# Kernel optimization log

Hardware: AMD Instinct MI355X
Metric: run time of the kernel (lower is better)

## Reference

```python
import jax, jax.numpy as jnp
import numpy as np

N_HASHES = 4
CHUNK = 144
REDUCTION = 4

# PyTorch bicubic (a=-0.75), align_corners=False, integer scale 2 ->
# fixed fractional offsets t=0.75 (even outputs) and t=0.25 (odd outputs).
_EW = jnp.array([-0.03515625, 0.26171875, 0.87890625, -0.10546875], jnp.float32)
_OW = _EW[::-1]


def _up2_axis(x, axis):
    n = x.shape[axis]
    pad = [(0, 0)] * x.ndim
    pad[axis] = (2, 2)
    xp = jnp.pad(x, pad, mode='edge')  # torch clamps border indices
    sl = lambda s: jax.lax.slice_in_dim(xp, s, s + n, axis=axis)
    even = sum(_EW[k] * sl(k) for k in range(4))
    odd = sum(_OW[k] * sl(k + 1) for k in range(4))
    out = jnp.stack([even, odd], axis=axis + 1)
    shp = list(x.shape)
    shp[axis] = 2 * n
    return out.reshape(shp)


def bicubic_up2(x):
    return _up2_axis(_up2_axis(x, 2), 3)


def conv2d(x, w, b, pad):
    y = jax.lax.conv_general_dilated(x, w, (1, 1), [(pad, pad), (pad, pad)],
                                     dimension_numbers=('NCHW', 'OIHW', 'NCHW'))
    return y + b[None, :, None, None]


def _adj(t):
    # attend to own + two adjacent buckets along chunk axis (axis=2)
    return jnp.concatenate([t, jnp.roll(t, 1, axis=2), jnp.roll(t, -1, axis=2)], axis=3)


def nlsa(x, wm, bm, wa, ba, rot):
    N, Cc, H, W = x.shape
    L = H * W
    xe = conv2d(x, wm, bm, 1).reshape(N, -1, L).transpose(0, 2, 1)  # [N,L,C]
    ye = conv2d(x, wa, ba, 0).reshape(N, -1, L).transpose(0, 2, 1)  # [N,L,C*red]
    C = xe.shape[-1]
    hash_buckets = min(L // CHUNK + (L // CHUNK) % 2, 128)
    # LSH: random rotations -> argmax bucket codes (non-differentiable, detached)
    rotated = jnp.einsum('btf,fhi->bhti', xe, rot)  # [N,h,L,hb//2]
    rotated = jnp.concatenate([rotated, -rotated], axis=-1)  # [N,h,L,hb]
    codes = jnp.argmax(rotated, axis=-1)  # [N,h,L]
    codes = codes + (jnp.arange(N_HASHES) * hash_buckets)[None, :, None]
    codes = jax.lax.stop_gradient(codes.reshape(N, -1))  # [N,h*L]
    indices = jnp.argsort(codes, axis=-1)
    undo = jnp.argsort(indices, axis=-1)
    mod = indices % L
    xs = jnp.take_along_axis(xe, mod[..., None], axis=1)  # [N,h*L,C]
    ys = jnp.take_along_axis(ye, mod[..., None], axis=1)  # [N,h*L,C*red]
    padding = (-L) % CHUNK
    xb = xs.reshape(N, N_HASHES, L, C)
    yb = ys.reshape(N, N_HASHES, L, C * REDUCTION)
    if padding:
        xb = jnp.concatenate([xb, xb[:, :, -padding:, :]], axis=2)
        yb = jnp.concatenate([yb, yb[:, :, -padding:, :]], axis=2)
    nch = xb.shape[2] // CHUNK
    xb = xb.reshape(N, N_HASHES, nch, CHUNK, C)
    yb = yb.reshape(N, N_HASHES, nch, CHUNK, C * REDUCTION)
    xm = xb / jnp.maximum(jnp.linalg.norm(xb, axis=-1, keepdims=True), 5e-5)
    xm = _adj(xm)      # [N,h,k,3*chunk,C]
    ybj = _adj(yb)     # [N,h,k,3*chunk,C*red]
    raw = jnp.einsum('bhkie,bhkje->bhkij', xb, xm)  # [N,h,k,chunk,3*chunk]
    bscore = jax.scipy.special.logsumexp(raw, axis=-1, keepdims=True)
    score = jnp.exp(raw - bscore)
    ret = jnp.einsum('bhkij,bhkje->bhkie', score, ybj)
    ret = ret.reshape(N, N_HASHES, -1, C * REDUCTION)
    bscore = bscore.reshape(N, N_HASHES, -1)
    if padding:
        ret = ret[:, :, :-padding]
        bscore = bscore[:, :, :-padding]
    ret = ret.reshape(N, -1, C * REDUCTION)
    bscore = bscore.reshape(N, -1)
    ret = jnp.take_along_axis(ret, undo[..., None], axis=1)
    bscore = jnp.take_along_axis(bscore, undo, axis=1)
    ret = ret.reshape(N, N_HASHES, L, C * REDUCTION)
    probs = jax.nn.softmax(bscore.reshape(N, N_HASHES, L, 1), axis=1)
    ret = jnp.sum(ret * probs, axis=1)  # [N,L,C*red]
    return ret.transpose(0, 2, 1).reshape(N, -1, H, W) + x


def setup_inputs() -> dict:
    key = jax.random.key(0)
    ks = jax.random.split(key, 8)
    w = lambda k, shape, fan: (jax.random.normal(k, shape, jnp.float32) / np.sqrt(fan)).astype(jnp.float32)
    return {
        'x': jax.random.normal(ks[0], (2, 64, 96, 96), jnp.float32),
        'w1': w(ks[1], (64, 64, 3, 3), 64 * 9), 'b1': jnp.zeros((64,), jnp.float32),
        'w2': w(ks[2], (64, 64, 3, 3), 64 * 9), 'b2': jnp.zeros((64,), jnp.float32),
        'wm': w(ks[3], (16, 64, 3, 3), 64 * 9), 'bm': jnp.zeros((16,), jnp.float32),
        'wa': w(ks[4], (64, 64, 1, 1), 64), 'ba': jnp.zeros((64,), jnp.float32),
        'rot': jax.random.normal(ks[5], (16, N_HASHES, 64), jnp.float32),  # [C, h, hash_buckets//2]
    }


def reference(x, w1, b1, w2, b2, wm, bm, wa, ba, rot):
    x = bicubic_up2(x)
    x = jax.nn.relu(conv2d(x, w1, b1, 1))
    x = jax.nn.relu(conv2d(x, w2, b2, 1))
    return nlsa(x, wm, bm, wa, ba, rot)
```

## Files before the change

kernel.cpp:

```cpp
#include <hip/hip_runtime.h>
#include <math.h>

#define NB 2
#define CIN 64
#define H0 96
#define W0 96
#define HH 192
#define WW 192
#define LL (HH*WW)
#define NHASH 4
#define CHK 144
#define NCHK 256
#define CE 16
#define CV 64
#define NBUCK 128
#define SEGL 576
#define NSEG 64

#define K_ROWB   80
#define V_ROWB   912
#define P_ROWB   72
#define KQ_SZB   34560
#define VT_SZB   58368
#define PST_SZB  10368
#define LKI_SZB  1728
#define QN_SZB   576
#define LDS_T1   (VT_SZB + PST_SZB + LKI_SZB)
#define LDS_T2   (KQ_SZB + VT_SZB + PST_SZB + LKI_SZB + QN_SZB)
#define CONV_LDS (2*4*66*64*2)

typedef __attribute__((ext_vector_type(8))) short short8_t;
typedef __attribute__((ext_vector_type(4))) float f32x4;
union FragU { unsigned int u[4]; int4 i; short8_t s; };

__device__ __forceinline__ unsigned int cvtpk_bf16(float a, float b){
  unsigned int r;
  asm("v_cvt_pk_bf16_f32 %0, %1, %2" : "=v"(r) : "v"(a), "v"(b));
  return r;
}
__device__ __forceinline__ float bfl(unsigned int u){ return __uint_as_float(u << 16); }
__device__ __forceinline__ float bfh(unsigned int u){ return __uint_as_float(u & 0xffff0000u); }

__global__ __launch_bounds__(256) void k_upsample(const float* __restrict__ x,
                                                  float* __restrict__ out){
  int idx = blockIdx.x*256 + threadIdx.x;
  if (idx >= NB*CIN*HH*WW) return;
  int ox = idx % WW; int t2 = idx / WW;
  int oy = t2 % HH;  t2 /= HH;
  int i = oy >> 1, a = oy & 1;
  int j = ox >> 1, b = ox & 1;
  const float e0=-0.03515625f, e1=0.26171875f, e2=0.87890625f, e3=-0.10546875f;
  float wy[4], wx[4]; int ty[4], tx[4];
  if (a){ wy[0]=e3; wy[1]=e2; wy[2]=e1; wy[3]=e0; } else { wy[0]=e0; wy[1]=e1; wy[2]=e2; wy[3]=e3; }
  if (b){ wx[0]=e3; wx[1]=e2; wx[2]=e1; wx[3]=e0; } else { wx[0]=e0; wx[1]=e1; wx[2]=e2; wx[3]=e3; }
  int offy = a ? -1 : -2, offx = b ? -1 : -2;
  #pragma unroll
  for (int k=0;k<4;k++){
    int t = i + offy + k; ty[k] = t<0?0:(t>H0-1?H0-1:t);
    int s = j + offx + k; tx[k] = s<0?0:(s>W0-1?W0-1:s);
  }
  const float* xp = x + (size_t)t2*H0*W0;
  float s = 0.f;
  #pragma unroll
  for (int ky=0;ky<4;ky++){
    const float* row = xp + ty[ky]*W0;
    float rs = 0.f;
    rs = fmaf(wx[0], row[tx[0]], rs);
    rs = fmaf(wx[1], row[tx[1]], rs);
    rs = fmaf(wx[2], row[tx[2]], rs);
    rs = fmaf(wx[3], row[tx[3]], rs);
    s = fmaf(wy[ky], rs, s);
  }
  out[idx] = s;
}

__global__ __launch_bounds__(256) void k_prepw(const float* __restrict__ w,
    unsigned short* __restrict__ wsT, int CO){
  int idx = blockIdx.x*256 + threadIdx.x;
  if (idx >= CO*64*9) return;
  int tap = idx % 9; int rem = idx / 9;
  int ci = rem % 64; int co = rem / 64;
  float v = w[(size_t)(co*64 + ci)*9 + tap];
  unsigned int hu = cvtpk_bf16(v, v) & 0xffffu;
  float hf = bfl(hu);
  unsigned int lu = cvtpk_bf16(v - hf, 0.f) & 0xffffu;
  int half = ci >> 5, kg = (ci >> 3) & 3, e = ci & 7;
  size_t base = ((size_t)(tap*2 + half)*2)*CO*32 + ((size_t)co*4 + kg)*8 + e;
  wsT[base]         = (unsigned short)hu;
  wsT[base + (size_t)CO*32] = (unsigned short)lu;
}

template<int CO, bool RELU, bool OUT_NLC>
__global__ __launch_bounds__(256) void k_conv3m(const float* __restrict__ in,
    const unsigned short* __restrict__ wsT, const float* __restrict__ bias,
    float* __restrict__ out){
  extern __shared__ char cvsm[];
  unsigned short (*inH)[66][64] = (unsigned short (*)[66][64])cvsm;
  unsigned short (*inL)[66][64] = (unsigned short (*)[66][64])(cvsm + 4*66*64*2);
  const int t = threadIdx.x;
  const int bx = blockIdx.x, by = blockIdx.y, n = blockIdx.z;
  const int y0 = by*2;
  const int x0 = bx*64;
  const int l = t & 63, w = t >> 6;
  const int lq = l & 15, kg = l >> 4;

  for (int e = t; e < 4096; e += 256){
    const int chunk = e & 15;
    const int strip = e >> 4;
    const int ci = strip & 63, row = strip >> 6;
    const int gy = y0 + row - 1;
    float4 v = make_float4(0.f,0.f,0.f,0.f);
    if (gy >= 0 && gy < HH)
      v = *(const float4*)&in[(((size_t)n*CIN + ci)*HH + gy)*WW + x0 + chunk*4];
    float vv[4] = {v.x, v.y, v.z, v.w};
    #pragma unroll
    for (int j = 0; j < 4; ++j){
      const int col = 1 + chunk*4 + j;
      const int sci = (((ci >> 3) ^ (col & 7)) << 3) | (ci & 7);
      unsigned int hu = cvtpk_bf16(vv[j], vv[j]);
      unsigned int lu = cvtpk_bf16(vv[j] - bfl(hu), 0.f);
      inH[row][col][sci] = (unsigned short)hu;
      inL[row][col][sci] = (unsigned short)lu;
    }
  }
  {
    const int ci = t & 63, row = t >> 6;
    const int gy = y0 + row - 1;
    const bool okY = (gy >= 0 && gy < HH);
    const float* ip = &in[(((size_t)n*CIN + ci)*HH + (size_t)(okY?gy:0))*WW];
    float vL = (okY && x0 >= 1) ? ip[x0-1] : 0.f;
    float vR = (okY && x0+64 < WW) ? ip[x0+64] : 0.f;
    unsigned int hL = cvtpk_bf16(vL, vL);
    unsigned int lLu = cvtpk_bf16(vL - bfl(hL), 0.f);
    unsigned int hR = cvtpk_bf16(vR, vR);
    unsigned int lRu = cvtpk_bf16(vR - bfl(hR), 0.f);
    const int sci0 = ci;
    const int sci65 = (((ci >> 3) ^ 1) << 3) | (ci & 7);
    inH[row][0][sci0]  = (unsigned short)hL;  inL[row][0][sci0]  = (unsigned short)lLu;
    inH[row][65][sci65] = (unsigned short)hR; inL[row][65][sci65] = (unsigned short)lRu;
  }
  __syncthreads();

  constexpr int NCT = CO/16;
  f32x4 acc0[NCT], acc1[NCT];
  #pragma unroll
  for (int c=0;c<NCT;c++){ acc0[c] = (f32x4){0.f,0.f,0.f,0.f}; acc1[c] = acc0[c]; }
  const unsigned short* wlane = wsT + (size_t)lq*32 + (size_t)kg*8;

  #pragma unroll
  for (int tap=0; tap<9; ++tap){
    const int ky = tap/3, kx = tap - ky*3;
    const int col = w*16 + lq + kx;
    #pragma unroll
    for (int half=0; half<2; ++half){
      const int sci = ((((half<<2) | kg) ^ (col & 7)) << 3);
      FragU Bh0, Bl0, Bh1, Bl1;
      Bh0.i = *(const int4*)&inH[ky  ][col][sci];
      Bl0.i = *(const int4*)&inL[ky  ][col][sci];
      Bh1.i = *(const int4*)&inH[ky+1][col][sci];
      Bl1.i = *(const int4*)&inL[ky+1][col][sci];
      const unsigned short* wth = wlane + (size_t)((tap*2+half)*2)*CO*32;
      #pragma unroll
      for (int ct=0; ct<NCT; ++ct){
        FragU Ah, Al;
        Ah.i = *(const int4*)(wth + ct*512);
        Al.i = *(const int4*)(wth + CO*32 + ct*512);
        acc0[ct] = __builtin_amdgcn_mfma_f32_16x16x32_bf16(Ah.s, Bl0.s, acc0[ct], 0,0,0);
        acc0[ct] = __builtin_amdgcn_mfma_f32_16x16x32_bf16(Al.s, Bh0.s, acc0[ct], 0,0,0);
        acc0[ct] = __builtin_amdgcn_mfma_f32_16x16x32_bf16(Ah.s, Bh0.s, acc0[ct], 0,0,0);
        acc1[ct] = __builtin_amdgcn_mfma_f32_16x16x32_bf16(Ah.s, Bl1.s, acc1[ct], 0,0,0);
        acc1[ct] = __builtin_amdgcn_mfma_f32_16x16x32_bf16(Al.s, Bh1.s, acc1[ct], 0,0,0);
        acc1[ct] = __builtin_amdgcn_mfma_f32_16x16x32_bf16(Ah.s, Bh1.s, acc1[ct], 0,0,0);
      }
    }
  }

  const int px = x0 + w*16 + lq;
  if constexpr (!OUT_NLC){
    #pragma unroll
    for (int ct=0; ct<NCT; ++ct){
      #pragma unroll
      for (int r=0; r<4; ++r){
        const int co = ct*16 + kg*4 + r;
        const float bv = bias[co];
        float v0 = acc0[ct][r] + bv;
        float v1 = acc1[ct][r] + bv;
        if (RELU){ v0 = fmaxf(v0, 0.f); v1 = fmaxf(v1, 0.f); }
        out[(((size_t)n*CO + co)*HH + y0  )*WW + px] = v0;
        out[(((size_t)n*CO + co)*HH + y0+1)*WW + px] = v1;
      }
    }
  } else {
    #pragma unroll
    for (int r=0; r<4; ++r){
      const int co = kg*4 + r;
      const float bv = bias[co];
      float v0 = acc0[0][r] + bv;
      float v1 = acc1[0][r] + bv;
      if (RELU){ v0 = fmaxf(v0, 0.f); v1 = fmaxf(v1, 0.f); }
      out[((size_t)n*LL + (y0  )*WW + px)*CO + co] = v0;
      out[((size_t)n*LL + (y0+1)*WW + px)*CO + co] = v1;
    }
  }
}

__global__ __launch_bounds__(256) void k_conv1x1(const float* __restrict__ x2,
    const float* __restrict__ wa, const float* __restrict__ ba,
    unsigned short* __restrict__ yeB){
  __shared__ float xs[64][64];
  __shared__ float wts[64][64];
  const int t = threadIdx.x;
  const int n = blockIdx.y;
  const int l0 = blockIdx.x*64;
  for (int e=t; e<4096; e+=256){
    int ci = e >> 6, l = e & 63;
    xs[ci][l]  = x2[((size_t)n*CIN+ci)*LL + l0 + l];
    wts[ci][l] = wa[(size_t)l*64 + ci];
  }
  __syncthreads();
  const int l = t & 63, cq = t >> 6;
  float acc[16];
  #pragma unroll
  for (int i=0;i<16;i++) acc[i] = ba[cq*16+i];
  for (int ci=0; ci<64; ci++){
    float xv = xs[ci][l];
    #pragma unroll
    for (int i=0;i<16;i++) acc[i] = fmaf(xv, wts[ci][cq*16+i], acc[i]);
  }
  unsigned int wds[8];
  #pragma unroll
  for (int i=0;i<8;i++) wds[i] = cvtpk_bf16(acc[2*i], acc[2*i+1]);
  uint4* op = (uint4*)&yeB[((size_t)n*LL + l0 + l)*64 + cq*16];
  op[0] = make_uint4(wds[0],wds[1],wds[2],wds[3]);
  op[1] = make_uint4(wds[4],wds[5],wds[6],wds[7]);
}

__global__ __launch_bounds__(128) void k_codes(const float* __restrict__ xe,
    const float* __restrict__ rot, unsigned char* __restrict__ codes){
  __shared__ float rs[NHASH][64][16];
  const int t = threadIdx.x;
  for (int e=t; e<4096; e+=128){
    int f = e >> 8; int rem = e & 255;
    int h = rem >> 6; int i = rem & 63;
    rs[h][i][f] = rot[((size_t)f*NHASH + h)*64 + i];
  }
  __syncthreads();
  const int n = blockIdx.y;
  const int l = blockIdx.x*128 + t;
  float q[16];
  const float* xr = &xe[((size_t)n*LL + l)*16];
  #pragma unroll
  for (int f=0;f<16;f++) q[f] = xr[f];
  #pragma unroll
  for (int h=0;h<NHASH;h++){
    float bp = -3.0e38f, bn = -3.0e38f; int ap=0, an=0;
    for (int i=0;i<64;i++){
      float s = 0.f;
      #pragma unroll
      for (int f=0;f<16;f++) s = fmaf(q[f], rs[h][i][f], s);
      if (s > bp){ bp = s; ap = i; }
      if (-s > bn){ bn = -s; an = i; }
    }
    int code = (bp >= bn) ? ap : (64 + an);
    codes[((size_t)n*NHASH + h)*LL + l] = (unsigned char)code;
  }
}

__global__ __launch_bounds__(256) void k_hist(const unsigned char* __restrict__ codes,
    unsigned int* __restrict__ segHist){
  __shared__ unsigned int h[NBUCK];
  const int t = threadIdx.x;
  if (t < NBUCK) h[t] = 0;
  __syncthreads();
  const int n = blockIdx.z, hh = blockIdx.y, s = blockIdx.x;
  const unsigned char* cp = codes + ((size_t)n*NHASH + hh)*LL + (size_t)s*SEGL;
  for (int e=t; e<SEGL; e+=256) atomicAdd(&h[cp[e]], 1u);
  __syncthreads();
  if (t < NBUCK)
    segHist[(((size_t)(n*NHASH+hh))*NSEG + s)*NBUCK + t] = h[t];
}

__global__ __launch_bounds__(128) void k_scan(unsigned int* __restrict__ segHist){
  __shared__ unsigned int tot[NBUCK];
  __shared__ unsigned int base[NBUCK];
  const int b = threadIdx.x;
  const size_t off = (size_t)blockIdx.x * NSEG * NBUCK;
  unsigned int run = 0;
  for (int s=0;s<NSEG;s++){
    unsigned int v = segHist[off + (size_t)s*NBUCK + b];
    segHist[off + (size_t)s*NBUCK + b] = run;
    run += v;
  }
  tot[b] = run;
  __syncthreads();
  if (b==0){ unsigned int r=0; for (int i=0;i<NBUCK;i++){ base[i]=r; r+=tot[i]; } }
  __syncthreads();
  const unsigned int bb = base[b];
  for (int s=0;s<NSEG;s++) segHist[off + (size_t)s*NBUCK + b] += bb;
}

__global__ __launch_bounds__(256) void k_rank(const unsigned char* __restrict__ codes,
    const unsigned int* __restrict__ segHist, int* __restrict__ sortPos,
    int* __restrict__ srtIdx){
  __shared__ unsigned int cw[SEGL/4];
  __shared__ unsigned int sbase[NBUCK];
  const int t = threadIdx.x;
  const int n = blockIdx.z, hh = blockIdx.y, s = blockIdx.x;
  const size_t cb = ((size_t)n*NHASH + hh)*LL + (size_t)s*SEGL;
  const unsigned int* cp32 = (const unsigned int*)(codes + cb);
  for (int e=t; e<SEGL/4; e+=256) cw[e] = cp32[e];
  if (t < NBUCK)
    sbase[t] = segHist[(((size_t)(n*NHASH+hh))*NSEG + s)*NBUCK + t];
  __syncthreads();
  const size_t ob = ((size_t)n*NHASH + hh)*LL;
  for (int e=t; e<SEGL; e+=256){
    unsigned int c = (cw[e>>2] >> ((e&3)*8)) & 0xffu;
    unsigned int mul = c * 0x01010101u;
    int cnt = 0;
    const int nw = e >> 2;
    for (int wi=0; wi<nw; wi++){
      unsigned int v = cw[wi] ^ mul;
      unsigned int t1 = (v & 0x7f7f7f7fu) + 0x7f7f7f7fu;
      unsigned int z = ~(t1 | v) & 0x80808080u;
      cnt += __popc(z);
    }
    unsigned int lastw = cw[nw];
    const int nbp = e & 3;
    for (int bp=0; bp<nbp; bp++)
      if (((lastw >> (bp*8)) & 0xffu) == c) cnt++;
    int pos = (int)sbase[c] + cnt;
    int l = s*SEGL + e;
    sortPos[ob + l] = pos;
    srtIdx[ob + pos] = l;
  }
}

__global__ __launch_bounds__(256) void k_gatherK(const float* __restrict__ xe,
    const int* __restrict__ srtIdx, unsigned short* __restrict__ Ksrt,
    float* __restrict__ normQ){
  const int idx = blockIdx.x*256 + threadIdx.x;
  if (idx >= NB*NHASH*LL) return;
  const int n = idx / (NHASH*LL);
  const int lk = srtIdx[idx];
  const float4* xr = (const float4*)&xe[((size_t)n*LL + lk)*16];
  float4 v0 = xr[0], v1 = xr[1], v2 = xr[2], v3 = xr[3];
  float f[16] = {v0.x,v0.y,v0.z,v0.w, v1.x,v1.y,v1.z,v1.w,
                 v2.x,v2.y,v2.z,v2.w, v3.x,v3.y,v3.z,v3.w};
  float ss = 0.f;
  #pragma unroll
  for (int i=0;i<16;i++) ss = fmaf(f[i], f[i], ss);
  const float nq = sqrtf(ss);
  normQ[idx] = nq;
  const float inv = 1.f / fmaxf(nq, 5e-5f);
  #pragma unroll
  for (int i=0;i<16;i++) f[i] *= inv;
  unsigned int kh[8], klo[8];
  #pragma unroll
  for (int i=0;i<8;i++) kh[i] = cvtpk_bf16(f[2*i], f[2*i+1]);
  #pragma unroll
  for (int i=0;i<8;i++)
    klo[i] = cvtpk_bf16(f[2*i] - bfl(kh[i]), f[2*i+1] - bfh(kh[i]));
  int4* kr = (int4*)(Ksrt + (size_t)idx*32);
  kr[0] = make_int4((int)kh[0],(int)kh[1],(int)kh[2],(int)kh[3]);
  kr[1] = make_int4((int)kh[4],(int)kh[5],(int)kh[6],(int)kh[7]);
  kr[2] = make_int4((int)klo[0],(int)klo[1],(int)klo[2],(int)klo[3]);
  kr[3] = make_int4((int)klo[4],(int)klo[5],(int)klo[6],(int)klo[7]);
}

template<int TIER>
__global__ __launch_bounds__(576) void k_attn2(const float* __restrict__ xe,
    const unsigned short* __restrict__ yeB, const int* __restrict__ srtIdx,
    const unsigned short* __restrict__ Ksrt, const float* __restrict__ normQ,
    unsigned short* __restrict__ retS, float* __restrict__ bscore){
  extern __shared__ char smem[];
  constexpr int KQOFF = (TIER==2) ? KQ_SZB : 0;
  unsigned short* Kq = (unsigned short*)smem;
  char* Vt  = smem + KQOFF;
  char* Pst = Vt + VT_SZB;
  int* lkI  = (int*)(Pst + PST_SZB);
  float* qn = (float*)(Pst + PST_SZB + LKI_SZB);

  const int t = threadIdx.x;
  const int k = blockIdx.x, hh = blockIdx.y, n = blockIdx.z;
  const size_t sb = ((size_t)n*NHASH + hh)*LL;
  const int l = t & 63, w = t >> 6;
  const int lq16 = l & 15, g = l >> 4;

  if (t < 432){
    const int c3 = t / CHK, jl = t - c3*CHK;
    const int kc = (c3==0) ? k : ((c3==1) ? ((k+NCHK-1)&(NCHK-1)) : ((k+1)&(NCHK-1)));
    const int lk = srtIdx[sb + (size_t)kc*CHK + jl];
    lkI[t] = lk;
    if constexpr (TIER==2){
      const float4* xr = (const float4*)&xe[((size_t)n*LL + lk)*16];
      float4 v0 = xr[0], v1 = xr[1], v2 = xr[2], v3 = xr[3];
      float f[16] = {v0.x,v0.y,v0.z,v0.w, v1.x,v1.y,v1.z,v1.w,
                     v2.x,v2.y,v2.z,v2.w, v3.x,v3.y,v3.z,v3.w};
      float ss = 0.f;
      #pragma unroll
      for (int i=0;i<16;i++) ss = fmaf(f[i], f[i], ss);
      const float nq = sqrtf(ss);
      if (c3 == 0) qn[jl] = nq;
      const float inv = 1.f / fmaxf(nq, 5e-5f);
      #pragma unroll
      for (int i=0;i<16;i++) f[i] *= inv;
      unsigned int kh[8], klo[8];
      #pragma unroll
      for (int i=0;i<8;i++) kh[i] = cvtpk_bf16(f[2*i], f[2*i+1]);
      #pragma unroll
      for (int i=0;i<8;i++)
        klo[i] = cvtpk_bf16(f[2*i] - bfl(kh[i]), f[2*i+1] - bfh(kh[i]));
      int4* kr = (int4*)((char*)Kq + t*K_ROWB);
      kr[0] = make_int4((int)kh[0],(int)kh[1],(int)kh[2],(int)kh[3]);
      kr[1] = make_int4((int)kh[4],(int)kh[5],(int)kh[6],(int)kh[7]);
      kr[2] = make_int4((int)klo[0],(int)klo[1],(int)klo[2],(int)klo[3]);
      kr[3] = make_int4((int)klo[4],(int)klo[5],(int)klo[6],(int)klo[7]);
    }
  }
  if (t < 512){
    int c = t >> 3, jp = t & 7;
    *(unsigned int*)(Vt + c*V_ROWB + 864 + jp*4) = 0u;
  }
  __syncthreads();

  #pragma unroll 4
  for (int it=0; it<24; ++it){
    const int e = t + it*576;
    const int jp = e >> 6, c = e & 63;
    const unsigned int a = yeB[((size_t)n*LL + lkI[2*jp  ])*64 + c];
    const unsigned int b = yeB[((size_t)n*LL + lkI[2*jp+1])*64 + c];
    *(unsigned int*)(Vt + c*V_ROWB + jp*4) = a | (b << 16);
  }
  const int qg = w*16 + lq16;
  const int pq = k*CHK + qg;
  FragU b1, b2;
  float nq_;
  if constexpr (TIER==1){
    const unsigned short* qrow = Ksrt + (sb + pq)*32;
    b1.i = *(const int4*)(qrow + (g&1)*8);
    if (g < 2) b2.i = *(const int4*)(qrow + 16 + (g&1)*8);
    else { b2.u[0]=0u; b2.u[1]=0u; b2.u[2]=0u; b2.u[3]=0u; }
    nq_ = normQ[sb + pq];
  } else {
    const char* qrow = (const char*)Kq + qg*K_ROWB;
    b1.i = *(const int4*)(qrow + (g&1)*16);
    if (g < 2) b2.i = *(const int4*)(qrow + 32 + (g&1)*16);
    else { b2.u[0]=0u; b2.u[1]=0u; b2.u[2]=0u; b2.u[3]=0u; }
    nq_ = qn[qg];
  }
  const float msc = fmaxf(nq_, 5e-5f);
  __syncthreads();

  float sum = 0.f;
  f32x4 O0 = {0.f,0.f,0.f,0.f}, O1 = O0, O2 = O0, O3 = O0;
  char* Pw = Pst + w*(16*P_ROWB);
  for (int u=0; u<14; ++u){
    #pragma unroll
    for (int sub=0; sub<2; ++sub){
      const int t27 = u*2 + sub;
      uint2 pw;
      if (t27 < 27){
        FragU a;
        if constexpr (TIER==1){
          const int c3 = t27 / 9;
          const int kc = (c3==0) ? k : ((c3==1) ? ((k+NCHK-1)&(NCHK-1)) : ((k+1)&(NCHK-1)));
          const int row16 = (t27 - c3*9)*16;
          a.i = *(const int4*)(Ksrt + (sb + (size_t)kc*CHK + row16 + lq16)*32 + g*8);
        } else {
          a.i = *(const int4*)((const char*)Kq + (size_t)(t27*16 + lq16)*K_ROWB + g*16);
        }
        f32x4 C = {0.f,0.f,0.f,0.f};
        C = __builtin_amdgcn_mfma_f32_16x16x32_bf16(a.s, b2.s, C, 0, 0, 0);
        C = __builtin_amdgcn_mfma_f32_16x16x32_bf16(a.s, b1.s, C, 0, 0, 0);
        const float p0 = __expf(fmaf(msc, C[0], -nq_));
        const float p1 = __expf(fmaf(msc, C[1], -nq_));
        const float p2 = __expf(fmaf(msc, C[2], -nq_));
        const float p3 = __expf(fmaf(msc, C[3], -nq_));
        sum += (p0+p1) + (p2+p3);
        pw = make_uint2(cvtpk_bf16(p0,p1), cvtpk_bf16(p2,p3));
      } else {
        pw = make_uint2(0u, 0u);
      }
      *(uint2*)(Pw + lq16*P_ROWB + sub*32 + g*8) = pw;
    }
    asm volatile("s_waitcnt lgkmcnt(0)" ::: "memory");
    __builtin_amdgcn_sched_barrier(0);
    FragU bp; bp.i = *(const int4*)(Pw + lq16*P_ROWB + g*16);
    const char* Vb = Vt + lq16*V_ROWB + u*64 + g*16;
    FragU av;
    av.i = *(const int4*)(Vb);             O0 = __builtin_amdgcn_mfma_f32_16x16x32_bf16(av.s, bp.s, O0, 0,0,0);
    av.i = *(const int4*)(Vb + 16*V_ROWB); O1 = __builtin_amdgcn_mfma_f32_16x16x32_bf16(av.s, bp.s, O1, 0,0,0);
    av.i = *(const int4*)(Vb + 32*V_ROWB); O2 = __builtin_amdgcn_mfma_f32_16x16x32_bf16(av.s, bp.s, O2, 0,0,0);
    av.i = *(const int4*)(Vb + 48*V_ROWB); O3 = __builtin_amdgcn_mfma_f32_16x16x32_bf16(av.s, bp.s, O3, 0,0,0);
  }
  sum += __shfl_xor(sum, 16);
  sum += __shfl_xor(sum, 32);
  const float linv = 1.f / sum;

  unsigned short* op = &retS[(sb + pq)*64];
  {
    uint2 s0 = make_uint2(cvtpk_bf16(O0[0]*linv, O0[1]*linv), cvtpk_bf16(O0[2]*linv, O0[3]*linv));
    uint2 s1 = make_uint2(cvtpk_bf16(O1[0]*linv, O1[1]*linv), cvtpk_bf16(O1[2]*linv, O1[3]*linv));
    uint2 s2 = make_uint2(cvtpk_bf16(O2[0]*linv, O2[1]*linv), cvtpk_bf16(O2[2]*linv, O2[3]*linv));
    uint2 s3 = make_uint2(cvtpk_bf16(O3[0]*linv, O3[1]*linv), cvtpk_bf16(O3[2]*linv, O3[3]*linv));
    *(uint2*)(op +  0 + g*4) = s0;
    *(uint2*)(op + 16 + g*4) = s1;
    *(uint2*)(op + 32 + g*4) = s2;
    *(uint2*)(op + 48 + g*4) = s3;
  }
  if (g == 0) bscore[sb + pq] = nq_ + logf(sum);
}

__global__ __launch_bounds__(256) void k_combine(const unsigned short* __restrict__ retS,
    const float* __restrict__ bscore, const int* __restrict__ sortPos,
    const float* __restrict__ x2, float* __restrict__ out){
  const int idx = blockIdx.x*256 + threadIdx.x;
  if (idx >= NB*LL) return;
  const int l = idx % LL, n = idx / LL;
  float bs[NHASH]; int pp[NHASH];
  #pragma unroll
  for (int h=0;h<NHASH;h++){
    size_t sb = ((size_t)n*NHASH + h)*LL;
    int p = sortPos[sb + l];
    pp[h] = p; bs[h] = bscore[sb + p];
  }
  float m = fmaxf(fmaxf(bs[0],bs[1]), fmaxf(bs[2],bs[3]));
  float wsum = 0.f; float wv[NHASH];
  #pragma unroll
  for (int h=0;h<NHASH;h++){ wv[h] = expf(bs[h]-m); wsum += wv[h]; }
  const float winv = 1.f / wsum;
  float o[64];
  #pragma unroll
  for (int i=0;i<64;i++) o[i]=0.f;
  #pragma unroll
  for (int h=0;h<NHASH;h++){
    const float wh = wv[h]*winv;
    const uint4* rp = (const uint4*)&retS[(((size_t)n*NHASH + h)*LL + pp[h])*64];
    #pragma unroll
    for (int i2=0;i2<8;i2++){
      uint4 v = rp[i2];
      o[i2*8+0] = fmaf(wh, bfl(v.x), o[i2*8+0]);
      o[i2*8+1] = fmaf(wh, bfh(v.x), o[i2*8+1]);
      o[i2*8+2] = fmaf(wh, bfl(v.y), o[i2*8+2]);
      o[i2*8+3] = fmaf(wh, bfh(v.y), o[i2*8+3]);
      o[i2*8+4] = fmaf(wh, bfl(v.z), o[i2*8+4]);
      o[i2*8+5] = fmaf(wh, bfh(v.z), o[i2*8+5]);
      o[i2*8+6] = fmaf(wh, bfl(v.w), o[i2*8+6]);
      o[i2*8+7] = fmaf(wh, bfh(v.w), o[i2*8+7]);
    }
  }
  #pragma unroll
  for (int c=0;c<64;c++){
    size_t oi = ((size_t)n*64 + c)*LL + l;
    out[oi] = o[c] + x2[oi];
  }
}

extern "C" void kernel_launch(void* const* d_in, const int* in_sizes, int n_in,
                              void* d_out, int out_size, void* d_ws, size_t ws_size,
                              hipStream_t stream){
  const float* x   = (const float*)d_in[0];
  const float* w1  = (const float*)d_in[1];
  const float* b1  = (const float*)d_in[2];
  const float* w2  = (const float*)d_in[3];
  const float* b2  = (const float*)d_in[4];
  const float* wm  = (const float*)d_in[5];
  const float* bm  = (const float*)d_in[6];
  const float* wa  = (const float*)d_in[7];
  const float* ba  = (const float*)d_in[8];
  const float* rot = (const float*)d_in[9];
  float* outp = (float*)d_out;
  char* ws = (char*)d_ws;
  const size_t FM   = (size_t)NB*CIN*HH*WW*sizeof(float);
  const size_t YEB  = (size_t)NB*LL*64*2;
  const size_t RETB = (size_t)NB*NHASH*LL*64*2;
  const size_t NHL4 = (size_t)NB*NHASH*LL*4;

  char* p = ws;
  unsigned short* yeB = (unsigned short*)p;  p += YEB;
  char* regA = p;                            p += RETB;
  float* x2  = (float*)p;                    p += FM;
  float* xe  = (float*)p;                    p += (size_t)NB*LL*CE*sizeof(float);
  unsigned char* codes = (unsigned char*)p;  p += (size_t)NB*NHASH*LL;
  unsigned int* segHist = (unsigned int*)p;  p += (size_t)NB*NHASH*NSEG*NBUCK*4;
  int* sortPos = (int*)p;                    p += NHL4;
  int* srtIdx  = (int*)p;                    p += NHL4;
  float* bscore = (float*)p;                 p += NHL4;
  unsigned short* wsT1 = (unsigned short*)p; p += (size_t)9*2*2*64*32*2;
  unsigned short* wsT2 = (unsigned short*)p; p += (size_t)9*2*2*64*32*2;
  unsigned short* wsTm = (unsigned short*)p; p += (size_t)9*2*2*16*32*2;
  const size_t needT2 = (size_t)(p - ws);
  unsigned short* Ksrt = (unsigned short*)p; p += (size_t)NB*NHASH*LL*32*2;
  float* normQ = (float*)p;                  p += NHL4;
  const size_t needT1 = (size_t)(p - ws);

  unsigned short* retS = (unsigned short*)regA;
  float* x0u = (float*)regA;
  float* y1  = (float*)(regA + FM);
  if (ws_size < needT2) return;
  const bool preg = (ws_size >= needT1);

  hipFuncSetAttribute((const void*)k_attn2<1>,
                      hipFuncAttributeMaxDynamicSharedMemorySize, LDS_T1);
  hipFuncSetAttribute((const void*)k_attn2<2>,
                      hipFuncAttributeMaxDynamicSharedMemorySize, LDS_T2);
  hipFuncSetAttribute((const void*)k_conv3m<64,true,false>,
                      hipFuncAttributeMaxDynamicSharedMemorySize, CONV_LDS);
  hipFuncSetAttribute((const void*)k_conv3m<16,false,true>,
                      hipFuncAttributeMaxDynamicSharedMemorySize, CONV_LDS);

  k_prepw<<<dim3((64*64*9+255)/256), dim3(256), 0, stream>>>(w1, wsT1, 64);
  k_prepw<<<dim3((64*64*9+255)/256), dim3(256), 0, stream>>>(w2, wsT2, 64);
  k_prepw<<<dim3((16*64*9+255)/256), dim3(256), 0, stream>>>(wm, wsTm, 16);
  k_upsample<<<dim3((NB*CIN*HH*WW+255)/256), dim3(256), 0, stream>>>(x, x0u);
  k_conv3m<64,true,false><<<dim3(3, HH/2, NB), dim3(256), CONV_LDS, stream>>>(x0u, wsT1, b1, y1);
  k_conv3m<64,true,false><<<dim3(3, HH/2, NB), dim3(256), CONV_LDS, stream>>>(y1, wsT2, b2, x2);
  k_conv3m<16,false,true><<<dim3(3, HH/2, NB), dim3(256), CONV_LDS, stream>>>(x2, wsTm, bm, xe);
  k_conv1x1<<<dim3(LL/64, NB), dim3(256), 0, stream>>>(x2, wa, ba, yeB);
  k_codes<<<dim3(LL/128, NB), dim3(128), 0, stream>>>(xe, rot, codes);
  k_hist<<<dim3(NSEG, NHASH, NB), dim3(256), 0, stream>>>(codes, segHist);
  k_scan<<<dim3(NB*NHASH), dim3(128), 0, stream>>>(segHist);
  k_rank<<<dim3(NSEG, NHASH, NB), dim3(256), 0, stream>>>(codes, segHist, sortPos, srtIdx);
  if (preg){
    k_gatherK<<<dim3((NB*NHASH*LL+255)/256), dim3(256), 0, stream>>>(xe, srtIdx, Ksrt, normQ);
    k_attn2<1><<<dim3(NCHK, NHASH, NB), dim3(576), LDS_T1, stream>>>(
        xe, yeB, srtIdx, Ksrt, normQ, retS, bscore);
  } else {
    k_attn2<2><<<dim3(NCHK, NHASH, NB), dim3(576), LDS_T2, stream>>>(
        xe, yeB, srtIdx, Ksrt, normQ, retS, bscore);
  }
  k_combine<<<dim3((NB*LL+255)/256), dim3(256), 0, stream>>>(retS, bscore, sortPos, x2, outp);
}
```

Measured before the change: 355.2 us.

## Keep conv activations as padded NHWC bf16 hi/lo planes between stages

The upsample and 3x3 convs now write zero-padded channel-last bf16 hi/lo pairs with the LDS swizzle already applied. Each conv then loads its tile with straight 16-byte copies instead of converting fp32 NCHW data and handling borders per block. x2 is also stored channel-last, with the 1x1 conv and combine adjusted to match, and the fallback attention tier is removed. The cost is an extra border-zeroing kernel, reuse of the Ksrt workspace as a ping-pong buffer, and a larger minimum workspace requirement.

```diff
diff --git a/kernel.cpp b/kernel.cpp
--- a/kernel.cpp
+++ b/kernel.cpp
@@ -12,21 +12,19 @@
 #define CHK 144
 #define NCHK 256
 #define CE 16
-#define CV 64
 #define NBUCK 128
 #define SEGL 576
 #define NSEG 64
+#define PW 194
+#define PS ((size_t)NB*PW*PW*64)
 
 #define K_ROWB   80
 #define V_ROWB   912
 #define P_ROWB   72
-#define KQ_SZB   34560
 #define VT_SZB   58368
 #define PST_SZB  10368
 #define LKI_SZB  1728
-#define QN_SZB   576
 #define LDS_T1   (VT_SZB + PST_SZB + LKI_SZB)
-#define LDS_T2   (KQ_SZB + VT_SZB + PST_SZB + LKI_SZB + QN_SZB)
 #define CONV_LDS (2*4*66*64*2)
 
 typedef __attribute__((ext_vector_type(8))) short short8_t;
@@ -41,37 +39,78 @@
 __device__ __forceinline__ float bfl(unsigned int u){ return __uint_as_float(u << 16); }
 __device__ __forceinline__ float bfh(unsigned int u){ return __uint_as_float(u & 0xffff0000u); }
 
-__global__ __launch_bounds__(256) void k_upsample(const float* __restrict__ x,
-                                                  float* __restrict__ out){
-  int idx = blockIdx.x*256 + threadIdx.x;
-  if (idx >= NB*CIN*HH*WW) return;
-  int ox = idx % WW; int t2 = idx / WW;
-  int oy = t2 % HH;  t2 /= HH;
-  int i = oy >> 1, a = oy & 1;
-  int j = ox >> 1, b = ox & 1;
+__global__ __launch_bounds__(256) void k_zerob(unsigned short* pA, unsigned short* pB){
+  const int cid = blockIdx.x*256 + threadIdx.x;
+  if (cid >= 4*2*772*8) return;
+  const int chunk = cid & 7;
+  int cell = cid >> 3;
+  const int plane = cell / (2*772); cell -= plane*(2*772);
+  const int n = cell / 772; int b = cell - n*772;
+  int ypad, xpad;
+  if (b < 194){ ypad = 0; xpad = b; }
+  else if (b < 388){ ypad = 193; xpad = b-194; }
+  else if (b < 580){ ypad = b-388+1; xpad = 0; }
+  else { ypad = b-580+1; xpad = 193; }
+  unsigned short* base = (plane < 2 ? pA : pB) + (size_t)(plane & 1)*PS;
+  *(uint4*)(base + (((size_t)n*PW + ypad)*PW + xpad)*64 + chunk*8) =
+      make_uint4(0u,0u,0u,0u);
+}
+
+__global__ __launch_bounds__(256) void k_upsample2(const float* __restrict__ x,
+    unsigned short* __restrict__ oh, unsigned short* __restrict__ ol){
+  __shared__ unsigned int pk[64][65];
+  const int t = threadIdx.x;
+  const int bx = blockIdx.x, oy = blockIdx.y, n = blockIdx.z;
+  const int oxl = t & 63, cq = t >> 6;
+  const int ox = bx*64 + oxl;
+  const int i = oy >> 1, a = oy & 1;
+  const int j = ox >> 1, b = ox & 1;
   const float e0=-0.03515625f, e1=0.26171875f, e2=0.87890625f, e3=-0.10546875f;
   float wy[4], wx[4]; int ty[4], tx[4];
   if (a){ wy[0]=e3; wy[1]=e2; wy[2]=e1; wy[3]=e0; } else { wy[0]=e0; wy[1]=e1; wy[2]=e2; wy[3]=e3; }
   if (b){ wx[0]=e3; wx[1]=e2; wx[2]=e1; wx[3]=e0; } else { wx[0]=e0; wx[1]=e1; wx[2]=e2; wx[3]=e3; }
-  int offy = a ? -1 : -2, offx = b ? -1 : -2;
+  const int offy = a ? -1 : -2, offx = b ? -1 : -2;
   #pragma unroll
   for (int k=0;k<4;k++){
-    int t = i + offy + k; ty[k] = t<0?0:(t>H0-1?H0-1:t);
+    int u = i + offy + k; ty[k] = u<0?0:(u>H0-1?H0-1:u);
     int s = j + offx + k; tx[k] = s<0?0:(s>W0-1?W0-1:s);
   }
-  const float* xp = x + (size_t)t2*H0*W0;
-  float s = 0.f;
-  #pragma unroll
-  for (int ky=0;ky<4;ky++){
-    const float* row = xp + ty[ky]*W0;
-    float rs = 0.f;
-    rs = fmaf(wx[0], row[tx[0]], rs);
-    rs = fmaf(wx[1], row[tx[1]], rs);
-    rs = fmaf(wx[2], row[tx[2]], rs);
-    rs = fmaf(wx[3], row[tx[3]], rs);
-    s = fmaf(wy[ky], rs, s);
-  }
-  out[idx] = s;
+  for (int ci = cq*16; ci < cq*16+16; ++ci){
+    const float* xp = x + ((size_t)n*CIN + ci)*(H0*W0);
+    float s = 0.f;
+    #pragma unroll
+    for (int ky=0;ky<4;ky++){
+      const float* row = xp + ty[ky]*W0;
+      float rs = 0.f;
+      rs = fmaf(wx[0], row[tx[0]], rs);
+      rs = fmaf(wx[1], row[tx[1]], rs);
+      rs = fmaf(wx[2], row[tx[2]], rs);
+      rs = fmaf(wx[3], row[tx[3]], rs);
+      s = fmaf(wy[ky], rs, s);
+    }
+    unsigned int hu = cvtpk_bf16(s, s);
+    unsigned int lu = cvtpk_bf16(s - bfl(hu), 0.f);
+    pk[oxl][ci] = (hu & 0xffffu) | (lu << 16);
+  }
+  __syncthreads();
+  const size_t rowb = (((size_t)n*PW + oy+1)*PW + bx*64 + 1)*64;
+  for (int e = t; e < 1024; e += 256){
+    const int plane = e >> 9, r2 = e & 511;
+    const int ox2 = r2 >> 3, c8 = r2 & 7;
+    const int xpad = bx*64 + ox2 + 1;
+    const int grp = (c8 ^ (xpad & 7))*8;
+    unsigned int a0=pk[ox2][grp+0], a1=pk[ox2][grp+1], a2=pk[ox2][grp+2], a3=pk[ox2][grp+3];
+    unsigned int a4=pk[ox2][grp+4], a5=pk[ox2][grp+5], a6=pk[ox2][grp+6], a7=pk[ox2][grp+7];
+    uint4 wv;
+    if (plane == 0){
+      wv.x = (a0&0xffffu)|(a1<<16); wv.y = (a2&0xffffu)|(a3<<16);
+      wv.z = (a4&0xffffu)|(a5<<16); wv.w = (a6&0xffffu)|(a7<<16);
+    } else {
+      wv.x = (a0>>16)|(a1&0xffff0000u); wv.y = (a2>>16)|(a3&0xffff0000u);
+      wv.z = (a4>>16)|(a5&0xffff0000u); wv.w = (a6>>16)|(a7&0xffff0000u);
+    }
+    *(uint4*)((plane ? ol : oh) + rowb + (size_t)ox2*64 + c8*8) = wv;
+  }
 }
 
 __global__ __launch_bounds__(256) void k_prepw(const float* __restrict__ w,
@@ -90,54 +129,28 @@
   wsT[base + (size_t)CO*32] = (unsigned short)lu;
 }
 
-template<int CO, bool RELU, bool OUT_NLC>
-__global__ __launch_bounds__(256) void k_conv3m(const float* __restrict__ in,
-    const unsigned short* __restrict__ wsT, const float* __restrict__ bias,
-    float* __restrict__ out){
+template<int CO, int OMODE>
+__global__ __launch_bounds__(256) void k_conv3s(const unsigned short* __restrict__ inh,
+    const unsigned short* __restrict__ inl, const unsigned short* __restrict__ wsT,
+    const float* __restrict__ bias, unsigned short* __restrict__ outh,
+    unsigned short* __restrict__ outl, float* __restrict__ outf){
   extern __shared__ char cvsm[];
   unsigned short (*inH)[66][64] = (unsigned short (*)[66][64])cvsm;
-  unsigned short (*inL)[66][64] = (unsigned short (*)[66][64])(cvsm + 4*66*64*2);
+  unsigned short (*inL)[66][64] = (unsigned short (*)[66][64])(cvsm + 33792);
   const int t = threadIdx.x;
   const int bx = blockIdx.x, by = blockIdx.y, n = blockIdx.z;
-  const int y0 = by*2;
-  const int x0 = bx*64;
+  const int y0 = by*2, x0 = bx*64;
   const int l = t & 63, w = t >> 6;
   const int lq = l & 15, kg = l >> 4;
 
-  for (int e = t; e < 4096; e += 256){
-    const int chunk = e & 15;
-    const int strip = e >> 4;
-    const int ci = strip & 63, row = strip >> 6;
-    const int gy = y0 + row - 1;
-    float4 v = make_float4(0.f,0.f,0.f,0.f);
-    if (gy >= 0 && gy < HH)
-      v = *(const float4*)&in[(((size_t)n*CIN + ci)*HH + gy)*WW + x0 + chunk*4];
-    float vv[4] = {v.x, v.y, v.z, v.w};
-    #pragma unroll
-    for (int j = 0; j < 4; ++j){
-      const int col = 1 + chunk*4 + j;
-      const int sci = (((ci >> 3) ^ (col & 7)) << 3) | (ci & 7);
-      unsigned int hu = cvtpk_bf16(vv[j], vv[j]);
-      unsigned int lu = cvtpk_bf16(vv[j] - bfl(hu), 0.f);
-      inH[row][col][sci] = (unsigned short)hu;
-      inL[row][col][sci] = (unsigned short)lu;
-    }
-  }
-  {
-    const int ci = t & 63, row = t >> 6;
-    const int gy = y0 + row - 1;
-    const bool okY = (gy >= 0 && gy < HH);
-    const float* ip = &in[(((size_t)n*CIN + ci)*HH + (size_t)(okY?gy:0))*WW];
-    float vL = (okY && x0 >= 1) ? ip[x0-1] : 0.f;
-    float vR = (okY && x0+64 < WW) ? ip[x0+64] : 0.f;
-    unsigned int hL = cvtpk_bf16(vL, vL);
-    unsigned int lLu = cvtpk_bf16(vL - bfl(hL), 0.f);
-    unsigned int hR = cvtpk_bf16(vR, vR);
-    unsigned int lRu = cvtpk_bf16(vR - bfl(hR), 0.f);
-    const int sci0 = ci;
-    const int sci65 = (((ci >> 3) ^ 1) << 3) | (ci & 7);
-    inH[row][0][sci0]  = (unsigned short)hL;  inL[row][0][sci0]  = (unsigned short)lLu;
-    inH[row][65][sci65] = (unsigned short)hR; inL[row][65][sci65] = (unsigned short)lRu;
+  const size_t gbase = (((size_t)n*PW + y0)*PW + x0)*64;
+  for (int e = t; e < 4224; e += 256){
+    const int plane = (e >= 2112);
+    const int rem = e - plane*2112;
+    const int row = rem / 528;
+    const int cw = rem - row*528;
+    const unsigned short* src = (plane ? inl : inh) + gbase + (size_t)row*(PW*64) + cw*8;
+    *(uint4*)(cvsm + plane*33792 + row*8448 + cw*16) = *(const uint4*)src;
   }
   __syncthreads();
 
@@ -176,30 +189,40 @@
   }
 
   const int px = x0 + w*16 + lq;
-  if constexpr (!OUT_NLC){
-    #pragma unroll
-    for (int ct=0; ct<NCT; ++ct){
-      #pragma unroll
-      for (int r=0; r<4; ++r){
-        const int co = ct*16 + kg*4 + r;
-        const float bv = bias[co];
-        float v0 = acc0[ct][r] + bv;
-        float v1 = acc1[ct][r] + bv;
-        if (RELU){ v0 = fmaxf(v0, 0.f); v1 = fmaxf(v1, 0.f); }
-        out[(((size_t)n*CO + co)*HH + y0  )*WW + px] = v0;
-        out[(((size_t)n*CO + co)*HH + y0+1)*WW + px] = v1;
-      }
-    }
-  } else {
+  const int xpad = px + 1;
+  const int xg = xpad & 7;
+  if constexpr (OMODE == 2){
     #pragma unroll
     for (int r=0; r<4; ++r){
       const int co = kg*4 + r;
       const float bv = bias[co];
-      float v0 = acc0[0][r] + bv;
-      float v1 = acc1[0][r] + bv;
-      if (RELU){ v0 = fmaxf(v0, 0.f); v1 = fmaxf(v1, 0.f); }
-      out[((size_t)n*LL + (y0  )*WW + px)*CO + co] = v0;
-      out[((size_t)n*LL + (y0+1)*WW + px)*CO + co] = v1;
+      outf[((size_t)n*LL + (size_t)(y0  )*WW + px)*16 + co] = acc0[0][r] + bv;
+      outf[((size_t)n*LL + (size_t)(y0+1)*WW + px)*16 + co] = acc1[0][r] + bv;
+    }
+  } else {
+    #pragma unroll
+    for (int ct=0; ct<NCT; ++ct){
+      const int ci = ct*16 + kg*4;
+      const int sgrp = (ct*2 + (kg>>1)) ^ xg;
+      #pragma unroll
+      for (int row=0; row<2; ++row){
+        const f32x4& A = row ? acc1[ct] : acc0[ct];
+        float v0 = fmaxf(A[0] + bias[ci+0], 0.f);
+        float v1 = fmaxf(A[1] + bias[ci+1], 0.f);
+        float v2 = fmaxf(A[2] + bias[ci+2], 0.f);
+        float v3 = fmaxf(A[3] + bias[ci+3], 0.f);
+        const unsigned int h0 = cvtpk_bf16(v0, v1);
+        const unsigned int h1 = cvtpk_bf16(v2, v3);
+        const unsigned int l0 = cvtpk_bf16(v0 - bfl(h0), v1 - bfh(h0));
+        const unsigned int l1 = cvtpk_bf16(v2 - bfl(h1), v3 - bfh(h1));
+        const size_t off = (((size_t)n*PW + (y0+row+1))*PW + xpad)*64 + sgrp*8 + (kg&1)*4;
+        *(uint2*)(outh + off) = make_uint2(h0, h1);
+        *(uint2*)(outl + off) = make_uint2(l0, l1);
+        if constexpr (OMODE == 1){
+          *(float4*)&outf[(((size_t)n*LL + (size_t)(y0+row)*WW + px)*64) + ci] =
+              make_float4(v0, v1, v2, v3);
+        }
+      }
     }
   }
 }
@@ -207,15 +230,15 @@
 __global__ __launch_bounds__(256) void k_conv1x1(const float* __restrict__ x2,
     const float* __restrict__ wa, const float* __restrict__ ba,
     unsigned short* __restrict__ yeB){
-  __shared__ float xs[64][64];
-  __shared__ float wts[64][64];
+  __shared__ float xs[64][65];
+  __shared__ float wts[64][65];
   const int t = threadIdx.x;
   const int n = blockIdx.y;
   const int l0 = blockIdx.x*64;
   for (int e=t; e<4096; e+=256){
-    int ci = e >> 6, l = e & 63;
-    xs[ci][l]  = x2[((size_t)n*CIN+ci)*LL + l0 + l];
-    wts[ci][l] = wa[(size_t)l*64 + ci];
+    int lv = e >> 6, ci = e & 63;
+    xs[ci][lv]  = x2[((size_t)n*LL + l0 + lv)*64 + ci];
+    wts[ci][lv] = wa[(size_t)lv*64 + ci];
   }
   __syncthreads();
   const int l = t & 63, cq = t >> 6;
@@ -329,9 +352,9 @@
     for (int bp=0; bp<nbp; bp++)
       if (((lastw >> (bp*8)) & 0xffu) == c) cnt++;
     int pos = (int)sbase[c] + cnt;
-    int l = s*SEGL + e;
-    sortPos[ob + l] = pos;
-    srtIdx[ob + pos] = l;
+    int lx = s*SEGL + e;
+    sortPos[ob + lx] = pos;
+    srtIdx[ob + pos] = lx;
   }
 }
 
@@ -367,18 +390,14 @@
   kr[3] = make_int4((int)klo[4],(int)klo[5],(int)klo[6],(int)klo[7]);
 }
 
-template<int TIER>
-__global__ __launch_bounds__(576) void k_attn2(const float* __restrict__ xe,
-    const unsigned short* __restrict__ yeB, const int* __restrict__ srtIdx,
-    const unsigned short* __restrict__ Ksrt, const float* __restrict__ normQ,
-    unsigned short* __restrict__ retS, float* __restrict__ bscore){
+__global__ __launch_bounds__(576) void k_attn2(const unsigned short* __restrict__ yeB,
+    const int* __restrict__ srtIdx, const unsigned short* __restrict__ Ksrt,
+    const float* __restrict__ normQ, unsigned short* __restrict__ retS,
+    float* __restrict__ bscore){
   extern __shared__ char smem[];
-  constexpr int KQOFF = (TIER==2) ? KQ_SZB : 0;
-  unsigned short* Kq = (unsigned short*)smem;
-  char* Vt  = smem + KQOFF;
+  char* Vt  = smem;
   char* Pst = Vt + VT_SZB;
   int* lkI  = (int*)(Pst + PST_SZB);
-  float* qn = (float*)(Pst + PST_SZB + LKI_SZB);
 
   const int t = threadIdx.x;
   const int k = blockIdx.x, hh = blockIdx.y, n = blockIdx.z;
@@ -389,33 +408,7 @@
   if (t < 432){
     const int c3 = t / CHK, jl = t - c3*CHK;
     const int kc = (c3==0) ? k : ((c3==1) ? ((k+NCHK-1)&(NCHK-1)) : ((k+1)&(NCHK-1)));
-    const int lk = srtIdx[sb + (size_t)kc*CHK + jl];
-    lkI[t] = lk;
-    if constexpr (TIER==2){
-      const float4* xr = (const float4*)&xe[((size_t)n*LL + lk)*16];
-      float4 v0 = xr[0], v1 = xr[1], v2 = xr[2], v3 = xr[3];
-      float f[16] = {v0.x,v0.y,v0.z,v0.w, v1.x,v1.y,v1.z,v1.w,
-                     v2.x,v2.y,v2.z,v2.w, v3.x,v3.y,v3.z,v3.w};
-      float ss = 0.f;
-      #pragma unroll
-      for (int i=0;i<16;i++) ss = fmaf(f[i], f[i], ss);
-      const float nq = sqrtf(ss);
-      if (c3 == 0) qn[jl] = nq;
-      const float inv = 1.f / fmaxf(nq, 5e-5f);
-      #pragma unroll
-      for (int i=0;i<16;i++) f[i] *= inv;
-      unsigned int kh[8], klo[8];
-      #pragma unroll
-      for (int i=0;i<8;i++) kh[i] = cvtpk_bf16(f[2*i], f[2*i+1]);
-      #pragma unroll
-      for (int i=0;i<8;i++)
-        klo[i] = cvtpk_bf16(f[2*i] - bfl(kh[i]), f[2*i+1] - bfh(kh[i]));
-      int4* kr = (int4*)((char*)Kq + t*K_ROWB);
-      kr[0] = make_int4((int)kh[0],(int)kh[1],(int)kh[2],(int)kh[3]);
-      kr[1] = make_int4((int)kh[4],(int)kh[5],(int)kh[6],(int)kh[7]);
-      kr[2] = make_int4((int)klo[0],(int)klo[1],(int)klo[2],(int)klo[3]);
-      kr[3] = make_int4((int)klo[4],(int)klo[5],(int)klo[6],(int)klo[7]);
-    }
+    lkI[t] = srtIdx[sb + (size_t)kc*CHK + jl];
   }
   if (t < 512){
     int c = t >> 3, jp = t & 7;
@@ -434,20 +427,11 @@
   const int qg = w*16 + lq16;
   const int pq = k*CHK + qg;
   FragU b1, b2;
-  float nq_;
-  if constexpr (TIER==1){
-    const unsigned short* qrow = Ksrt + (sb + pq)*32;
-    b1.i = *(const int4*)(qrow + (g&1)*8);
-    if (g < 2) b2.i = *(const int4*)(qrow + 16 + (g&1)*8);
-    else { b2.u[0]=0u; b2.u[1]=0u; b2.u[2]=0u; b2.u[3]=0u; }
-    nq_ = normQ[sb + pq];
-  } else {
-    const char* qrow = (const char*)Kq + qg*K_ROWB;
-    b1.i = *(const int4*)(qrow + (g&1)*16);
-    if (g < 2) b2.i = *(const int4*)(qrow + 32 + (g&1)*16);
-    else { b2.u[0]=0u; b2.u[1]=0u; b2.u[2]=0u; b2.u[3]=0u; }
-    nq_ = qn[qg];
-  }
+  const unsigned short* qrow = Ksrt + (sb + pq)*32;
+  b1.i = *(const int4*)(qrow + (g&1)*8);
+  if (g < 2) b2.i = *(const int4*)(qrow + 16 + (g&1)*8);
+  else { b2.u[0]=0u; b2.u[1]=0u; b2.u[2]=0u; b2.u[3]=0u; }
+  const float nq_ = normQ[sb + pq];
   const float msc = fmaxf(nq_, 5e-5f);
   __syncthreads();
 
@@ -460,15 +444,10 @@
       const int t27 = u*2 + sub;
       uint2 pw;
       if (t27 < 27){
-        FragU a;
-        if constexpr (TIER==1){
-          const int c3 = t27 / 9;
-          const int kc = (c3==0) ? k : ((c3==1) ? ((k+NCHK-1)&(NCHK-1)) : ((k+1)&(NCHK-1)));
-          const int row16 = (t27 - c3*9)*16;
-          a.i = *(const int4*)(Ksrt + (sb + (size_t)kc*CHK + row16 + lq16)*32 + g*8);
-        } else {
-          a.i = *(const int4*)((const char*)Kq + (size_t)(t27*16 + lq16)*K_ROWB + g*16);
-        }
+        const int c3 = t27 / 9;
+        const int kc = (c3==0) ? k : ((c3==1) ? ((k+NCHK-1)&(NCHK-1)) : ((k+1)&(NCHK-1)));
+        const int row16 = (t27 - c3*9)*16;
+        FragU a; a.i = *(const int4*)(Ksrt + (sb + (size_t)kc*CHK + row16 + lq16)*32 + g*8);
         f32x4 C = {0.f,0.f,0.f,0.f};
         C = __builtin_amdgcn_mfma_f32_16x16x32_bf16(a.s, b2.s, C, 0, 0, 0);
         C = __builtin_amdgcn_mfma_f32_16x16x32_bf16(a.s, b1.s, C, 0, 0, 0);
@@ -549,10 +528,14 @@
       o[i2*8+7] = fmaf(wh, bfh(v.w), o[i2*8+7]);
     }
   }
-  #pragma unroll
-  for (int c=0;c<64;c++){
-    size_t oi = ((size_t)n*64 + c)*LL + l;
-    out[oi] = o[c] + x2[oi];
+  const float4* xr = (const float4*)&x2[((size_t)n*LL + l)*64];
+  #pragma unroll
+  for (int c4=0; c4<16; ++c4){
+    float4 xv = xr[c4];
+    out[((size_t)n*64 + c4*4+0)*LL + l] = o[c4*4+0] + xv.x;
+    out[((size_t)n*64 + c4*4+1)*LL + l] = o[c4*4+1] + xv.y;
+    out[((size_t)n*64 + c4*4+2)*LL + l] = o[c4*4+2] + xv.z;
+    out[((size_t)n*64 + c4*4+3)*LL + l] = o[c4*4+3] + xv.w;
   }
 }
 
@@ -589,45 +572,42 @@
   unsigned short* wsT1 = (unsigned short*)p; p += (size_t)9*2*2*64*32*2;
   unsigned short* wsT2 = (unsigned short*)p; p += (size_t)9*2*2*64*32*2;
   unsigned short* wsTm = (unsigned short*)p; p += (size_t)9*2*2*16*32*2;
-  const size_t needT2 = (size_t)(p - ws);
   unsigned short* Ksrt = (unsigned short*)p; p += (size_t)NB*NHASH*LL*32*2;
   float* normQ = (float*)p;                  p += NHL4;
   const size_t needT1 = (size_t)(p - ws);
+  if (ws_size < needT1) return;
 
   unsigned short* retS = (unsigned short*)regA;
-  float* x0u = (float*)regA;
-  float* y1  = (float*)(regA + FM);
-  if (ws_size < needT2) return;
-  const bool preg = (ws_size >= needT1);
-
-  hipFuncSetAttribute((const void*)k_attn2<1>,
+  unsigned short* pairA = (unsigned short*)regA;
+  unsigned short* pairB = Ksrt;
+
+  hipFuncSetAttribute((const void*)k_attn2,
                       hipFuncAttributeMaxDynamicSharedMemorySize, LDS_T1);
-  hipFuncSetAttribute((const void*)k_attn2<2>,
-                      hipFuncAttributeMaxDynamicSharedMemorySize, LDS_T2);
-  hipFuncSetAttribute((const void*)k_conv3m<64,true,false>,
+  hipFuncSetAttribute((const void*)k_conv3s<64,0>,
                       hipFuncAttributeMaxDynamicSharedMemorySize, CONV_LDS);
-  hipFuncSetAttribute((const void*)k_conv3m<16,false,true>,
+  hipFuncSetAttribute((const void*)k_conv3s<64,1>,
+                      hipFuncAttributeMaxDynamicSharedMemorySize, CONV_LDS);
+  hipFuncSetAttribute((const void*)k_conv3s<16,2>,
                       hipFuncAttributeMaxDynamicSharedMemorySize, CONV_LDS);
 
   k_prepw<<<dim3((64*64*9+255)/256), dim3(256), 0, stream>>>(w1, wsT1, 64);
   k_prepw<<<dim3((64*64*9+255)/256), dim3(256), 0, stream>>>(w2, wsT2, 64);
   k_prepw<<<dim3((16*64*9+255)/256), dim3(256), 0, stream>>>(wm, wsTm, 16);
-  k_upsample<<<dim3((NB*CIN*HH*WW+255)/256), dim3(256), 0, stream>>>(x, x0u);
-  k_conv3m<64,true,false><<<dim3(3, HH/2, NB), dim3(256), CONV_LDS, stream>>>(x0u, wsT1, b1, y1);
-  k_conv3m<64,true,false><<<dim3(3, HH/2, NB), dim3(256), CONV_LDS, stream>>>(y1, wsT2, b2, x2);
-  k_conv3m<16,false,true><<<dim3(3, HH/2, NB), dim3(256), CONV_LDS, stream>>>(x2, wsTm, bm, xe);
+  k_zerob<<<dim3((4*2*772*8+255)/256), dim3(256), 0, stream>>>(pairA, pairB);
+  k_upsample2<<<dim3(WW/64, HH, NB), dim3(256), 0, stream>>>(x, pairA, pairA + PS);
+  k_conv3s<64,0><<<dim3(3, HH/2, NB), dim3(256), CONV_LDS, stream>>>(
+      pairA, pairA + PS, wsT1, b1, pairB, pairB + PS, nullptr);
+  k_conv3s<64,1><<<dim3(3, HH/2, NB), dim3(256), CONV_LDS, stream>>>(
+      pairB, pairB + PS, wsT2, b2, pairA, pairA + PS, x2);
+  k_conv3s<16,2><<<dim3(3, HH/2, NB), dim3(256), CONV_LDS, stream>>>(
+      pairA, pairA + PS, wsTm, bm, nullptr, nullptr, xe);
   k_conv1x1<<<dim3(LL/64, NB), dim3(256), 0, stream>>>(x2, wa, ba, yeB);
   k_codes<<<dim3(LL/128, NB), dim3(128), 0, stream>>>(xe, rot, codes);
   k_hist<<<dim3(NSEG, NHASH, NB), dim3(256), 0, stream>>>(codes, segHist);
   k_scan<<<dim3(NB*NHASH), dim3(128), 0, stream>>>(segHist);
   k_rank<<<dim3(NSEG, NHASH, NB), dim3(256), 0, stream>>>(codes, segHist, sortPos, srtIdx);
-  if (preg){
-    k_gatherK<<<dim3((NB*NHASH*LL+255)/256), dim3(256), 0, stream>>>(xe, srtIdx, Ksrt, normQ);
-    k_attn2<1><<<dim3(NCHK, NHASH, NB), dim3(576), LDS_T1, stream>>>(
-        xe, yeB, srtIdx, Ksrt, normQ, retS, bscore);
-  } else {
-    k_attn2<2><<<dim3(NCHK, NHASH, NB), dim3(576), LDS_T2, stream>>>(
-        xe, yeB, srtIdx, Ksrt, normQ, retS, bscore);
-  }
+  k_gatherK<<<dim3((NB*NHASH*LL+255)/256), dim3(256), 0, stream>>>(xe, srtIdx, Ksrt, normQ);
+  k_attn2<<<dim3(NCHK, NHASH, NB), dim3(576), LDS_T1, stream>>>(
+      yeB, srtIdx, Ksrt, normQ, retS, bscore);
   k_combine<<<dim3((NB*LL+255)/256), dim3(256), 0, stream>>>(retS, bscore, sortPos, x2, outp);
 }
```

Result: no change. 349.3 us (median of 2 runs) (-1.7%).
